# Performance work log

Measured on AMD Instinct MI355X. Metric: run time of the kernel, lower is better.

Reference implementation:

```python
import jax, jax.numpy as jnp
import numpy as np

D_MODEL = 1024
NUM_HEADS = 16
HEAD_DIM = D_MODEL // NUM_HEADS
B, S = 2, 2048


def setup_inputs() -> dict:
    key = jax.random.key(0)
    ks = jax.random.split(key, 10)
    sc = 1.0 / np.sqrt(D_MODEL)
    return {
        "x": jax.random.normal(ks[0], (B, S, D_MODEL), jnp.float32),
        "y": jax.random.normal(ks[1], (B, S, D_MODEL), jnp.float32),
        "Wkv": jax.random.normal(ks[2], (D_MODEL, 2 * D_MODEL), jnp.float32) * sc,
        "bkv": jax.random.normal(ks[3], (2 * D_MODEL,), jnp.float32) * 0.01,
        "Wq": jax.random.normal(ks[4], (D_MODEL, D_MODEL), jnp.float32) * sc,
        "bq": jax.random.normal(ks[5], (D_MODEL,), jnp.float32) * 0.01,
        "Wo": jax.random.normal(ks[6], (D_MODEL, D_MODEL), jnp.float32) * sc,
        "bo": jax.random.normal(ks[7], (D_MODEL,), jnp.float32) * 0.01,
    }


def reference(x, y, Wkv, bkv, Wq, bq, Wo, bo):
    b, s, d = x.shape
    # projections: kv from x (keys/values come from encoder side), q from y
    kv = x @ Wkv + bkv                      # [B, S, 2*d_model]
    q = y @ Wq + bq                         # [B, S, d_model]
    kv = kv.reshape(b, s, NUM_HEADS, 2 * HEAD_DIM).transpose(0, 2, 1, 3)  # [B,H,S,2*hd]
    q = q.reshape(b, s, NUM_HEADS, HEAD_DIM).transpose(0, 2, 1, 3)        # [B,H,S,hd]
    k, v = jnp.split(kv, 2, axis=-1)        # each [B,H,S,hd]
    scaled = jnp.einsum("bhqd,bhkd->bhqk", q, k) / np.sqrt(HEAD_DIM)      # [B,H,S,S]
    attention = jax.nn.softmax(scaled, axis=-1)
    values = jnp.einsum("bhqk,bhkd->bhqd", attention, v)                  # [B,H,S,hd]
    values = values.transpose(0, 2, 1, 3).reshape(b, s, d)                # [B,S,d_model]
    return values @ Wo + bo
```

## Files before the change

kernel.cpp:

```cpp
#include <hip/hip_runtime.h>
#include <hip/hip_bf16.h>

typedef __attribute__((ext_vector_type(8))) short short8;
typedef __attribute__((ext_vector_type(4))) short short4v;
typedef __attribute__((ext_vector_type(4))) float f32x4;

#define B_  2
#define S_  2048
#define H_  16
#define HD_ 64
#define D_  1024
#define QSCALE 0.18033688f

__device__ __forceinline__ short f2bs(float f) {
  union { float f; unsigned u; } c; c.f = f;
  unsigned u = c.u;
  u += 0x7fffu + ((u >> 16) & 1u);
  return (short)(u >> 16);
}

__device__ __forceinline__ float fexp2(float x) {
#if __has_builtin(__builtin_amdgcn_exp2f)
  return __builtin_amdgcn_exp2f(x);
#else
  return exp2f(x);
#endif
}

__device__ __forceinline__ float frcp(float x) {
#if __has_builtin(__builtin_amdgcn_rcpf)
  return __builtin_amdgcn_rcpf(x);
#else
  return 1.0f / x;
#endif
}

#define GL2LDS(gp, lp) __builtin_amdgcn_global_load_lds( \
    (const __attribute__((address_space(1))) unsigned int*)(gp), \
    (__attribute__((address_space(3))) unsigned int*)(lp), 16, 0, 0)

__global__ __launch_bounds__(256) void cvt2_kernel(const float* __restrict__ a,
                                                   const float* __restrict__ b,
                                                   short* __restrict__ oa,
                                                   short* __restrict__ ob, int n4each) {
  int i = blockIdx.x * 256 + threadIdx.x;
  const float4* src;
  short4v* dst;
  int j;
  if (i < n4each) { src = (const float4*)a; dst = (short4v*)oa; j = i; }
  else            { src = (const float4*)b; dst = (short4v*)ob; j = i - n4each; }
  float4 f = src[j];
  short4v o;
  o.x = f2bs(f.x); o.y = f2bs(f.y); o.z = f2bs(f.z); o.w = f2bs(f.w);
  dst[j] = o;
}

__global__ __launch_bounds__(256) void trcvt_kernel(const float* __restrict__ in,
                                                    short* __restrict__ out, int R, int C) {
  __shared__ float tile[64][65];
  const int tx = threadIdx.x & 63;
  const int ty = threadIdx.x >> 6;
  const int c0 = blockIdx.x * 64, r0 = blockIdx.y * 64;
#pragma unroll
  for (int i = 0; i < 16; ++i) {
    int r = ty + i * 4;
    tile[r][tx] = in[(size_t)(r0 + r) * C + c0 + tx];
  }
  __syncthreads();
#pragma unroll
  for (int i = 0; i < 16; ++i) {
    int r = ty + i * 4;
    out[(size_t)(c0 + r) * R + r0 + tx] = f2bs(tile[tx][r]);
  }
}

__global__ __launch_bounds__(256) void trcvt2_kernel(const float* __restrict__ in0, short* __restrict__ out0,
                                                     const float* __restrict__ in1, short* __restrict__ out1) {
  __shared__ float tile[64][65];
  const float* in = blockIdx.z ? in1 : in0;
  short* out = blockIdx.z ? out1 : out0;
  const int tx = threadIdx.x & 63;
  const int ty = threadIdx.x >> 6;
  const int c0 = blockIdx.x * 64, r0 = blockIdx.y * 64;
#pragma unroll
  for (int i = 0; i < 16; ++i) {
    int r = ty + i * 4;
    tile[r][tx] = in[(size_t)(r0 + r) * 1024 + c0 + tx];
  }
  __syncthreads();
#pragma unroll
  for (int i = 0; i < 16; ++i) {
    int r = ty + i * 4;
    out[(size_t)(c0 + r) * 1024 + r0 + tx] = f2bs(tile[tx][r]);
  }
}

template <int MODE>
__device__ __forceinline__ void gemm_body(const short* __restrict__ A, const short* __restrict__ Bt,
                                          const float* __restrict__ bias,
                                          void* __restrict__ out0, void* __restrict__ out1,
                                          int m0, int n0, int K,
                                          short* As, short* Bs) {
  const int tid = threadIdx.x;
  const int w = tid >> 6, lane = tid & 63;
  const int q15 = lane & 15, quad = lane >> 4;
  const int wm = (w >> 1) * 64, wn = (w & 1) * 64;

  f32x4 acc[4][4];
#pragma unroll
  for (int i = 0; i < 4; ++i)
#pragma unroll
    for (int j = 0; j < 4; ++j) acc[i][j] = f32x4{0.f, 0.f, 0.f, 0.f};

  const int srow = w * 16 + (lane >> 2);
  const int gch  = (lane & 3) ^ ((lane >> 3) & 3);
  const short* Ag = A + (size_t)(m0 + srow) * K + gch * 8;
  const short* Bg = Bt + (size_t)(n0 + srow) * K + gch * 8;
  short* Al = As + srow * 32 + (lane & 3) * 8;
  short* Bl = Bs + srow * 32 + (lane & 3) * 8;

  for (int kt = 0; kt < K; kt += 32) {
    GL2LDS(Ag + kt,                  Al);
    GL2LDS(Ag + kt + (size_t)64 * K, Al + 64 * 32);
    GL2LDS(Bg + kt,                  Bl);
    GL2LDS(Bg + kt + (size_t)64 * K, Bl + 64 * 32);
    __syncthreads();
    short8 af[4], bf[4];
#pragma unroll
    for (int mi = 0; mi < 4; ++mi) {
      int rr = wm + mi * 16 + q15;
      af[mi] = *(const short8*)(As + rr * 32 + ((quad ^ ((rr >> 1) & 3)) * 8));
    }
#pragma unroll
    for (int ni = 0; ni < 4; ++ni) {
      int rr = wn + ni * 16 + q15;
      bf[ni] = *(const short8*)(Bs + rr * 32 + ((quad ^ ((rr >> 1) & 3)) * 8));
    }
#pragma unroll
    for (int mi = 0; mi < 4; ++mi)
#pragma unroll
      for (int ni = 0; ni < 4; ++ni)
        acc[mi][ni] = __builtin_amdgcn_mfma_f32_16x16x32_bf16(af[mi], bf[ni], acc[mi][ni], 0, 0, 0);
    __syncthreads();
  }

#pragma unroll
  for (int mi = 0; mi < 4; ++mi) {
#pragma unroll
    for (int ni = 0; ni < 4; ++ni) {
      const int n = n0 + wn + ni * 16 + q15;
      const float bn = bias[n];
#pragma unroll
      for (int r = 0; r < 4; ++r) {
        const int m = m0 + wm + mi * 16 + quad * 4 + r;
        float v = acc[mi][ni][r] + bn;
        if constexpr (MODE == 0) {
          int b = m >> 11, s = m & 2047, hh = n >> 6, d = n & 63;
          ((short*)out0)[((size_t)((b * H_ + hh) * S_ + s) << 6) + d] = f2bs(v * QSCALE);
        } else {
          int b = m >> 11, s = m & 2047, hh = n >> 7, wi = n & 127;
          if (wi < 64)
            ((short*)out0)[((size_t)((b * H_ + hh) * S_ + s) << 6) + wi] = f2bs(v);
          else
            ((short*)out1)[((size_t)((b * H_ + hh) * HD_ + (wi - 64)) << 11) + s] = f2bs(v);
        }
      }
    }
  }
}

__global__ __launch_bounds__(256)
void proj_kernel(const short* __restrict__ xb, const short* __restrict__ Wkvt,
                 const float* __restrict__ bkv, short* __restrict__ Kb, short* __restrict__ Vtb,
                 const short* __restrict__ yb, const short* __restrict__ Wqt,
                 const float* __restrict__ bq, short* __restrict__ Qb) {
  __shared__ __align__(16) short As[128 * 32];
  __shared__ __align__(16) short Bs[128 * 32];
  int bx = blockIdx.x;
  if (bx < 512)
    gemm_body<1>(xb, Wkvt, bkv, Kb, Vtb, (bx >> 4) * 128, (bx & 15) * 128, 1024, As, Bs);
  else {
    bx -= 512;
    gemm_body<0>(yb, Wqt, bq, Qb, nullptr, (bx >> 3) * 128, (bx & 7) * 128, 1024, As, Bs);
  }
}

__global__ __launch_bounds__(256)
void gemm_o_kernel(const short* __restrict__ A, const short* __restrict__ Bt,
                   const float* __restrict__ bias, float* __restrict__ out) {
  __shared__ __align__(16) short As[64 * 32];
  __shared__ __align__(16) short Bs[128 * 32];
  const int tid = threadIdx.x;
  const int w = tid >> 6, lane = tid & 63;
  const int q15 = lane & 15, quad = lane >> 4;
  const int m0 = blockIdx.y * 64, n0 = blockIdx.x * 128;
  const int wm = (w >> 1) * 32, wn = (w & 1) * 64;

  f32x4 acc[2][4];
#pragma unroll
  for (int i = 0; i < 2; ++i)
#pragma unroll
    for (int j = 0; j < 4; ++j) acc[i][j] = f32x4{0.f, 0.f, 0.f, 0.f};

  const int raA = tid >> 2;
  const int gchA = (tid & 3) ^ ((tid >> 3) & 3);
  const short* Ag = A + (size_t)(m0 + raA) * 1024 + gchA * 8;
  short* Al = As + tid * 8;
  const int srow = w * 16 + (lane >> 2);
  const int gchB = (lane & 3) ^ ((lane >> 3) & 3);
  const short* Bg = Bt + (size_t)(n0 + srow) * 1024 + gchB * 8;
  short* Bl = Bs + srow * 32 + (lane & 3) * 8;

  for (int kt = 0; kt < 1024; kt += 32) {
    GL2LDS(Ag + kt,             Al);
    GL2LDS(Bg + kt,             Bl);
    GL2LDS(Bg + kt + 64 * 1024, Bl + 64 * 32);
    __syncthreads();
    short8 af[2], bf[4];
#pragma unroll
    for (int mi = 0; mi < 2; ++mi) {
      int rr = wm + mi * 16 + q15;
      af[mi] = *(const short8*)(As + rr * 32 + ((quad ^ ((rr >> 1) & 3)) * 8));
    }
#pragma unroll
    for (int ni = 0; ni < 4; ++ni) {
      int rr = wn + ni * 16 + q15;
      bf[ni] = *(const short8*)(Bs + rr * 32 + ((quad ^ ((rr >> 1) & 3)) * 8));
    }
#pragma unroll
    for (int mi = 0; mi < 2; ++mi)
#pragma unroll
      for (int ni = 0; ni < 4; ++ni)
        acc[mi][ni] = __builtin_amdgcn_mfma_f32_16x16x32_bf16(af[mi], bf[ni], acc[mi][ni], 0, 0, 0);
    __syncthreads();
  }

#pragma unroll
  for (int mi = 0; mi < 2; ++mi)
#pragma unroll
    for (int ni = 0; ni < 4; ++ni) {
      const int n = n0 + wn + ni * 16 + q15;
      const float bn = bias[n];
#pragma unroll
      for (int r = 0; r < 4; ++r) {
        const int m = m0 + wm + mi * 16 + quad * 4 + r;
        out[(size_t)m * 1024 + n] = acc[mi][ni][r] + bn;
      }
    }
}

#define PSTRIDE 72
__global__ __launch_bounds__(256)
void attn_kernel(const short* __restrict__ Q, const short* __restrict__ K,
                 const short* __restrict__ Vt, short* __restrict__ Out) {
  __shared__ __align__(16) short Qs[64 * 64];
  __shared__ __align__(16) short Ks[64 * 64];
  __shared__ __align__(16) short Vs[64 * 64];
  __shared__ __align__(16) short Ps[4][16 * PSTRIDE];
  const int tid = threadIdx.x;
  const int w = tid >> 6, lane = tid & 63;
  const int q15 = lane & 15, quad = lane >> 4;
  const int qt = blockIdx.x, h = blockIdx.y, b = blockIdx.z;
  const size_t bh = (size_t)(b * H_ + h);
  const short* Qg = Q + bh * (S_ * HD_) + qt * (64 * HD_);
  const short* Kg = K + bh * (S_ * HD_);
  const short* Vg = Vt + bh * (HD_ * S_);

  const int srow = w * 8 + (lane >> 3);
  const int gch  = (lane & 7) ^ (srow & 7);

  {
    const short* g = Qg + srow * 64 + gch * 8;
    short* l = Qs + w * 512 + lane * 8;
    GL2LDS(g, l);
    GL2LDS(g + 32 * 64, l + 2048);
  }
  __syncthreads();
  short8 aq[2];
  {
    const int rq = w * 16 + q15;
#pragma unroll
    for (int kk = 0; kk < 2; ++kk)
      aq[kk] = *(const short8*)(Qs + rq * 64 + (((kk * 4 + quad) ^ (q15 & 7)) * 8));
  }

  f32x4 oacc[4];
#pragma unroll
  for (int ni = 0; ni < 4; ++ni) oacc[ni] = f32x4{0.f, 0.f, 0.f, 0.f};
  float lsum[4] = {0.f, 0.f, 0.f, 0.f};

  const short* kg = Kg + srow * 64 + gch * 8;
  short* kl = Ks + w * 512 + lane * 8;
  const short* vg = Vg + (size_t)srow * S_ + gch * 8;
  short* vl = Vs + w * 512 + lane * 8;

  for (int kt = 0; kt < S_ / 64; ++kt) {
    __syncthreads();
    GL2LDS(kg + kt * 4096,        kl);
    GL2LDS(kg + kt * 4096 + 2048, kl + 2048);
    GL2LDS(vg + kt * 64,                   vl);
    GL2LDS(vg + kt * 64 + (size_t)32 * S_, vl + 32 * 64);
    __syncthreads();

    f32x4 sacc[4];
#pragma unroll
    for (int ni = 0; ni < 4; ++ni) sacc[ni] = f32x4{0.f, 0.f, 0.f, 0.f};
#pragma unroll
    for (int ni = 0; ni < 4; ++ni) {
      const int rr = ni * 16 + q15;
#pragma unroll
      for (int kk = 0; kk < 2; ++kk) {
        short8 bfr = *(const short8*)(Ks + rr * 64 + (((kk * 4 + quad) ^ (q15 & 7)) * 8));
        sacc[ni] = __builtin_amdgcn_mfma_f32_16x16x32_bf16(aq[kk], bfr, sacc[ni], 0, 0, 0);
      }
    }

#pragma unroll
    for (int ni = 0; ni < 4; ++ni)
#pragma unroll
      for (int r = 0; r < 4; ++r) {
        float p = fexp2(sacc[ni][r]);
        lsum[r] += p;
        Ps[w][(quad * 4 + r) * PSTRIDE + ni * 16 + q15] = f2bs(p);
      }

    short8 ap[2];
#pragma unroll
    for (int kk = 0; kk < 2; ++kk)
      ap[kk] = *(const short8*)(&Ps[w][q15 * PSTRIDE + kk * 32 + quad * 8]);
#pragma unroll
    for (int ni = 0; ni < 4; ++ni) {
      const int rr = ni * 16 + q15;
#pragma unroll
      for (int kk = 0; kk < 2; ++kk) {
        short8 bv = *(const short8*)(Vs + rr * 64 + (((kk * 4 + quad) ^ (q15 & 7)) * 8));
        oacc[ni] = __builtin_amdgcn_mfma_f32_16x16x32_bf16(ap[kk], bv, oacc[ni], 0, 0, 0);
      }
    }
  }

#pragma unroll
  for (int off = 1; off < 16; off <<= 1)
#pragma unroll
    for (int r = 0; r < 4; ++r)
      lsum[r] += __shfl_xor(lsum[r], off, 16);
  float inv[4];
#pragma unroll
  for (int r = 0; r < 4; ++r) inv[r] = frcp(lsum[r]);

#pragma unroll
  for (int ni = 0; ni < 4; ++ni) {
    const int col = h * HD_ + ni * 16 + q15;
#pragma unroll
    for (int r = 0; r < 4; ++r) {
      const int m = b * S_ + qt * 64 + w * 16 + quad * 4 + r;
      Out[(size_t)m * D_ + col] = f2bs(oacc[ni][r] * inv[r]);
    }
  }
}

extern "C" void kernel_launch(void* const* d_in, const int* in_sizes, int n_in,
                              void* d_out, int out_size, void* d_ws, size_t ws_size,
                              hipStream_t stream) {
  const float* x   = (const float*)d_in[0];
  const float* y   = (const float*)d_in[1];
  const float* Wkv = (const float*)d_in[2];
  const float* bkv = (const float*)d_in[3];
  const float* Wq  = (const float*)d_in[4];
  const float* bq  = (const float*)d_in[5];
  const float* Wo  = (const float*)d_in[6];
  const float* bo  = (const float*)d_in[7];
  float* out = (float*)d_out;

  short* xb   = (short*)d_ws;
  short* yb   = xb + (4 << 20);
  short* Wkvt = yb + (4 << 20);
  short* Wqt  = Wkvt + (2 << 20);
  short* Wot  = Wqt + (1 << 20);
  short* Kb   = Wot + (1 << 20);
  short* Vtb  = Kb + (4 << 20);
  short* Qb   = Vtb + (4 << 20);
  short* AOb  = Qb + (4 << 20);

  cvt2_kernel<<<8192, 256, 0, stream>>>(x, y, xb, yb, 1 << 20);
  trcvt_kernel<<<dim3(32, 16), 256, 0, stream>>>(Wkv, Wkvt, 1024, 2048);
  trcvt2_kernel<<<dim3(16, 16, 2), 256, 0, stream>>>(Wq, Wqt, Wo, Wot);

  proj_kernel<<<768, 256, 0, stream>>>(xb, Wkvt, bkv, Kb, Vtb, yb, Wqt, bq, Qb);
  attn_kernel<<<dim3(32, 16, 2), 256, 0, stream>>>(Qb, Kb, Vtb, AOb);
  gemm_o_kernel<<<dim3(8, 64), 256, 0, stream>>>(AOb, Wot, bo, out);
}
```

Measured before the change: 238.2 us.

## Stage V-transpose through LDS, swap QK MFMA operands, remap attention blocks per XCD

The KV projection epilogue now writes the transposed V tile through LDS so global stores are coalesced 16-byte writes instead of scattered 2-byte stores. The attention kernel swaps the QK^T MFMA operands so each lane holds a column of scores. That lets P be packed into bf16 pairs with vector LDS stores and the row sum reduced with fewer shuffles. Attention blocks are remapped so each XCD handles whole (batch, head) pairs, which should improve L2 reuse of K and V, and LDS is shared between Q and P. The output GEMM uses a smaller 64x64 tile to launch more blocks, at the cost of less reuse per block.

```diff
diff --git a/kernel.cpp b/kernel.cpp
--- a/kernel.cpp
+++ b/kernel.cpp
@@ -17,6 +17,11 @@
   unsigned u = c.u;
   u += 0x7fffu + ((u >> 16) & 1u);
   return (short)(u >> 16);
+}
+
+__device__ __forceinline__ unsigned pack_bf16(float a, float b) {
+  __hip_bfloat162 h = __float22bfloat162_rn(float2{a, b});
+  return *reinterpret_cast<unsigned*>(&h);
 }
 
 __device__ __forceinline__ float fexp2(float x) {
@@ -99,8 +104,9 @@
 __device__ __forceinline__ void gemm_body(const short* __restrict__ A, const short* __restrict__ Bt,
                                           const float* __restrict__ bias,
                                           void* __restrict__ out0, void* __restrict__ out1,
-                                          int m0, int n0, int K,
-                                          short* As, short* Bs) {
+                                          int m0, int n0, int K, short* smem) {
+  short* As = smem;
+  short* Bs = smem + 4096;
   const int tid = threadIdx.x;
   const int w = tid >> 6, lane = tid & 63;
   const int q15 = lane & 15, quad = lane >> 4;
@@ -144,27 +150,68 @@
     __syncthreads();
   }
 
-#pragma unroll
-  for (int mi = 0; mi < 4; ++mi) {
-#pragma unroll
-    for (int ni = 0; ni < 4; ++ni) {
-      const int n = n0 + wn + ni * 16 + q15;
-      const float bn = bias[n];
-#pragma unroll
-      for (int r = 0; r < 4; ++r) {
-        const int m = m0 + wm + mi * 16 + quad * 4 + r;
-        float v = acc[mi][ni][r] + bn;
-        if constexpr (MODE == 0) {
+  if constexpr (MODE == 0) {
+#pragma unroll
+    for (int mi = 0; mi < 4; ++mi)
+#pragma unroll
+      for (int ni = 0; ni < 4; ++ni) {
+        const int n = n0 + wn + ni * 16 + q15;
+        const float bn = bias[n];
+#pragma unroll
+        for (int r = 0; r < 4; ++r) {
+          const int m = m0 + wm + mi * 16 + quad * 4 + r;
           int b = m >> 11, s = m & 2047, hh = n >> 6, d = n & 63;
-          ((short*)out0)[((size_t)((b * H_ + hh) * S_ + s) << 6) + d] = f2bs(v * QSCALE);
-        } else {
-          int b = m >> 11, s = m & 2047, hh = n >> 7, wi = n & 127;
-          if (wi < 64)
-            ((short*)out0)[((size_t)((b * H_ + hh) * S_ + s) << 6) + wi] = f2bs(v);
-          else
-            ((short*)out1)[((size_t)((b * H_ + hh) * HD_ + (wi - 64)) << 11) + s] = f2bs(v);
+          ((short*)out0)[((size_t)((b * H_ + hh) * S_ + s) << 6) + d] = f2bs((acc[mi][ni][r] + bn) * QSCALE);
         }
       }
+  } else {
+    const int hh = n0 >> 7;
+    const int bb = m0 >> 11;
+    const size_t bh = (size_t)(bb * H_ + hh);
+    const int s0 = m0 & 2047;
+    if ((w & 1) == 0) {
+#pragma unroll
+      for (int mi = 0; mi < 4; ++mi)
+#pragma unroll
+        for (int ni = 0; ni < 4; ++ni) {
+          const float bn = bias[n0 + ni * 16 + q15];
+#pragma unroll
+          for (int r = 0; r < 4; ++r) {
+            const int s = s0 + wm + mi * 16 + quad * 4 + r;
+            ((short*)out0)[((bh * S_ + s) << 6) + ni * 16 + q15] = f2bs(acc[mi][ni][r] + bn);
+          }
+        }
+    } else {
+      short* VT = smem;
+#pragma unroll
+      for (int mi = 0; mi < 4; ++mi)
+#pragma unroll
+        for (int ni = 0; ni < 4; ++ni) {
+          const int d = ni * 16 + q15;
+          const float bn = bias[n0 + 64 + ni * 16 + q15];
+#pragma unroll
+          for (int t = 0; t < 2; ++t) {
+            const int chunk = (wm >> 1) + mi * 8 + quad * 2 + t;
+            unsigned pk = pack_bf16(acc[mi][ni][2 * t] + bn, acc[mi][ni][2 * t + 1] + bn);
+            *reinterpret_cast<unsigned*>(VT + d * 128 + ((chunk ^ (d & 15)) * 2)) = pk;
+          }
+        }
+    }
+    __syncthreads();
+    {
+      short* VT = smem;
+      const int d = tid >> 2, t4 = tid & 3;
+      unsigned vals[16];
+#pragma unroll
+      for (int c = 0; c < 16; ++c) {
+        int chunk = t4 * 16 + c;
+        vals[c] = *reinterpret_cast<unsigned*>(VT + d * 128 + ((chunk ^ (d & 15)) * 2));
+      }
+      uint4* dst = (uint4*)((short*)out1 + ((bh * HD_ + d) << 11) + s0 + t4 * 32);
+      dst[0] = uint4{vals[0], vals[1], vals[2], vals[3]};
+      dst[1] = uint4{vals[4], vals[5], vals[6], vals[7]};
+      dst[2] = uint4{vals[8], vals[9], vals[10], vals[11]};
+      dst[3] = uint4{vals[12], vals[13], vals[14], vals[15]};
     }
   }
 }
@@ -174,63 +221,59 @@
                  const float* __restrict__ bkv, short* __restrict__ Kb, short* __restrict__ Vtb,
                  const short* __restrict__ yb, const short* __restrict__ Wqt,
                  const float* __restrict__ bq, short* __restrict__ Qb) {
-  __shared__ __align__(16) short As[128 * 32];
-  __shared__ __align__(16) short Bs[128 * 32];
+  __shared__ __align__(16) short smem[8192];
   int bx = blockIdx.x;
   if (bx < 512)
-    gemm_body<1>(xb, Wkvt, bkv, Kb, Vtb, (bx >> 4) * 128, (bx & 15) * 128, 1024, As, Bs);
+    gemm_body<1>(xb, Wkvt, bkv, Kb, Vtb, (bx >> 4) * 128, (bx & 15) * 128, 1024, smem);
   else {
     bx -= 512;
-    gemm_body<0>(yb, Wqt, bq, Qb, nullptr, (bx >> 3) * 128, (bx & 7) * 128, 1024, As, Bs);
+    gemm_body<0>(yb, Wqt, bq, Qb, nullptr, (bx >> 3) * 128, (bx & 7) * 128, 1024, smem);
   }
 }
 
 __global__ __launch_bounds__(256)
 void gemm_o_kernel(const short* __restrict__ A, const short* __restrict__ Bt,
                    const float* __restrict__ bias, float* __restrict__ out) {
-  __shared__ __align__(16) short As[64 * 32];
-  __shared__ __align__(16) short Bs[128 * 32];
+  __shared__ __align__(16) short As[2048];
+  __shared__ __align__(16) short Bs[2048];
   const int tid = threadIdx.x;
   const int w = tid >> 6, lane = tid & 63;
   const int q15 = lane & 15, quad = lane >> 4;
-  const int m0 = blockIdx.y * 64, n0 = blockIdx.x * 128;
-  const int wm = (w >> 1) * 32, wn = (w & 1) * 64;
-
-  f32x4 acc[2][4];
+  const int m0 = blockIdx.y * 64, n0 = blockIdx.x * 64;
+  const int wm = (w >> 1) * 32, wn = (w & 1) * 32;
+
+  f32x4 acc[2][2];
 #pragma unroll
   for (int i = 0; i < 2; ++i)
 #pragma unroll
-    for (int j = 0; j < 4; ++j) acc[i][j] = f32x4{0.f, 0.f, 0.f, 0.f};
-
-  const int raA = tid >> 2;
-  const int gchA = (tid & 3) ^ ((tid >> 3) & 3);
-  const short* Ag = A + (size_t)(m0 + raA) * 1024 + gchA * 8;
+    for (int j = 0; j < 2; ++j) acc[i][j] = f32x4{0.f, 0.f, 0.f, 0.f};
+
+  const int row = tid >> 2;
+  const int gch = (tid & 3) ^ ((tid >> 3) & 3);
+  const short* Ag = A + (size_t)(m0 + row) * 1024 + gch * 8;
+  const short* Bg = Bt + (size_t)(n0 + row) * 1024 + gch * 8;
   short* Al = As + tid * 8;
-  const int srow = w * 16 + (lane >> 2);
-  const int gchB = (lane & 3) ^ ((lane >> 3) & 3);
-  const short* Bg = Bt + (size_t)(n0 + srow) * 1024 + gchB * 8;
-  short* Bl = Bs + srow * 32 + (lane & 3) * 8;
+  short* Bl = Bs + tid * 8;
 
   for (int kt = 0; kt < 1024; kt += 32) {
-    GL2LDS(Ag + kt,             Al);
-    GL2LDS(Bg + kt,             Bl);
-    GL2LDS(Bg + kt + 64 * 1024, Bl + 64 * 32);
-    __syncthreads();
-    short8 af[2], bf[4];
+    GL2LDS(Ag + kt, Al);
+    GL2LDS(Bg + kt, Bl);
+    __syncthreads();
+    short8 af[2], bf[2];
 #pragma unroll
     for (int mi = 0; mi < 2; ++mi) {
       int rr = wm + mi * 16 + q15;
       af[mi] = *(const short8*)(As + rr * 32 + ((quad ^ ((rr >> 1) & 3)) * 8));
     }
 #pragma unroll
-    for (int ni = 0; ni < 4; ++ni) {
+    for (int ni = 0; ni < 2; ++ni) {
       int rr = wn + ni * 16 + q15;
       bf[ni] = *(const short8*)(Bs + rr * 32 + ((quad ^ ((rr >> 1) & 3)) * 8));
     }
 #pragma unroll
     for (int mi = 0; mi < 2; ++mi)
 #pragma unroll
-      for (int ni = 0; ni < 4; ++ni)
+      for (int ni = 0; ni < 2; ++ni)
         acc[mi][ni] = __builtin_amdgcn_mfma_f32_16x16x32_bf16(af[mi], bf[ni], acc[mi][ni], 0, 0, 0);
     __syncthreads();
   }
@@ -238,7 +281,7 @@
 #pragma unroll
   for (int mi = 0; mi < 2; ++mi)
 #pragma unroll
-    for (int ni = 0; ni < 4; ++ni) {
+    for (int ni = 0; ni < 2; ++ni) {
       const int n = n0 + wn + ni * 16 + q15;
       const float bn = bias[n];
 #pragma unroll
@@ -249,18 +292,22 @@
     }
 }
 
-#define PSTRIDE 72
+#define PST 72
 __global__ __launch_bounds__(256)
 void attn_kernel(const short* __restrict__ Q, const short* __restrict__ K,
                  const short* __restrict__ Vt, short* __restrict__ Out) {
-  __shared__ __align__(16) short Qs[64 * 64];
-  __shared__ __align__(16) short Ks[64 * 64];
-  __shared__ __align__(16) short Vs[64 * 64];
-  __shared__ __align__(16) short Ps[4][16 * PSTRIDE];
+  __shared__ __align__(16) short lds[12800];
+  short* Ks = lds;
+  short* Vs = lds + 4096;
+  short* QP = lds + 8192;
   const int tid = threadIdx.x;
   const int w = tid >> 6, lane = tid & 63;
   const int q15 = lane & 15, quad = lane >> 4;
-  const int qt = blockIdx.x, h = blockIdx.y, b = blockIdx.z;
+  const int bx = blockIdx.x;
+  const int xcd = bx & 7, slot = bx >> 3;
+  const int pp = xcd * 4 + (slot >> 5);
+  const int qt = slot & 31;
+  const int h = pp & 15, b = pp >> 4;
   const size_t bh = (size_t)(b * H_ + h);
   const short* Qg = Q + bh * (S_ * HD_) + qt * (64 * HD_);
   const short* Kg = K + bh * (S_ * HD_);
@@ -271,7 +318,7 @@
 
   {
     const short* g = Qg + srow * 64 + gch * 8;
-    short* l = Qs + w * 512 + lane * 8;
+    short* l = QP + w * 512 + lane * 8;
     GL2LDS(g, l);
     GL2LDS(g + 32 * 64, l + 2048);
   }
@@ -281,13 +328,14 @@
     const int rq = w * 16 + q15;
 #pragma unroll
     for (int kk = 0; kk < 2; ++kk)
-      aq[kk] = *(const short8*)(Qs + rq * 64 + (((kk * 4 + quad) ^ (q15 & 7)) * 8));
-  }
+      aq[kk] = *(const short8*)(QP + rq * 64 + (((kk * 4 + quad) ^ (q15 & 7)) * 8));
+  }
+  short* Psw = QP + w * (16 * PST);
 
   f32x4 oacc[4];
 #pragma unroll
   for (int ni = 0; ni < 4; ++ni) oacc[ni] = f32x4{0.f, 0.f, 0.f, 0.f};
-  float lsum[4] = {0.f, 0.f, 0.f, 0.f};
+  float lsum = 0.f;
 
   const short* kg = Kg + srow * 64 + gch * 8;
   short* kl = Ks + w * 512 + lane * 8;
@@ -304,30 +352,32 @@
 
     f32x4 sacc[4];
 #pragma unroll
-    for (int ni = 0; ni < 4; ++ni) sacc[ni] = f32x4{0.f, 0.f, 0.f, 0.f};
-#pragma unroll
-    for (int ni = 0; ni < 4; ++ni) {
-      const int rr = ni * 16 + q15;
+    for (int mi = 0; mi < 4; ++mi) sacc[mi] = f32x4{0.f, 0.f, 0.f, 0.f};
+#pragma unroll
+    for (int mi = 0; mi < 4; ++mi) {
+      const int rr = mi * 16 + q15;
 #pragma unroll
       for (int kk = 0; kk < 2; ++kk) {
-        short8 bfr = *(const short8*)(Ks + rr * 64 + (((kk * 4 + quad) ^ (q15 & 7)) * 8));
-        sacc[ni] = __builtin_amdgcn_mfma_f32_16x16x32_bf16(aq[kk], bfr, sacc[ni], 0, 0, 0);
+        short8 ak = *(const short8*)(Ks + rr * 64 + (((kk * 4 + quad) ^ (q15 & 7)) * 8));
+        sacc[mi] = __builtin_amdgcn_mfma_f32_16x16x32_bf16(ak, aq[kk], sacc[mi], 0, 0, 0);
       }
     }
 
 #pragma unroll
-    for (int ni = 0; ni < 4; ++ni)
-#pragma unroll
-      for (int r = 0; r < 4; ++r) {
-        float p = fexp2(sacc[ni][r]);
-        lsum[r] += p;
-        Ps[w][(quad * 4 + r) * PSTRIDE + ni * 16 + q15] = f2bs(p);
-      }
+    for (int mi = 0; mi < 4; ++mi) {
+      float p0 = fexp2(sacc[mi][0]), p1 = fexp2(sacc[mi][1]);
+      float p2 = fexp2(sacc[mi][2]), p3 = fexp2(sacc[mi][3]);
+      lsum += (p0 + p1) + (p2 + p3);
+      uint2 pk;
+      pk.x = pack_bf16(p0, p1);
+      pk.y = pack_bf16(p2, p3);
+      *reinterpret_cast<uint2*>(Psw + q15 * PST + mi * 16 + quad * 4) = pk;
+    }
 
     short8 ap[2];
 #pragma unroll
     for (int kk = 0; kk < 2; ++kk)
-      ap[kk] = *(const short8*)(&Ps[w][q15 * PSTRIDE + kk * 32 + quad * 8]);
+      ap[kk] = *(const short8*)(Psw + q15 * PST + kk * 32 + quad * 8);
 #pragma unroll
     for (int ni = 0; ni < 4; ++ni) {
       const int rr = ni * 16 + q15;
@@ -339,14 +389,12 @@
     }
   }
 
-#pragma unroll
-  for (int off = 1; off < 16; off <<= 1)
-#pragma unroll
-    for (int r = 0; r < 4; ++r)
-      lsum[r] += __shfl_xor(lsum[r], off, 16);
+  lsum += __shfl_xor(lsum, 16);
+  lsum += __shfl_xor(lsum, 32);
   float inv[4];
 #pragma unroll
-  for (int r = 0; r < 4; ++r) inv[r] = frcp(lsum[r]);
+  for (int r = 0; r < 4; ++r)
+    inv[r] = frcp(__shfl(lsum, quad * 4 + r, 64));
 
 #pragma unroll
   for (int ni = 0; ni < 4; ++ni) {
@@ -387,6 +435,6 @@
   trcvt2_kernel<<<dim3(16, 16, 2), 256, 0, stream>>>(Wq, Wqt, Wo, Wot);
 
   proj_kernel<<<768, 256, 0, stream>>>(xb, Wkvt, bkv, Kb, Vtb, yb, Wqt, bq, Qb);
-  attn_kernel<<<dim3(32, 16, 2), 256, 0, stream>>>(Qb, Kb, Vtb, AOb);
-  gemm_o_kernel<<<dim3(8, 64), 256, 0, stream>>>(AOb, Wot, bo, out);
-}
+  attn_kernel<<<1024, 256, 0, stream>>>(Qb, Kb, Vtb, AOb);
+  gemm_o_kernel<<<dim3(16, 64), 256, 0, stream>>>(AOb, Wot, bo, out);
+}
```

After: 222.5 us. 1.07x faster.
